# Kernel tuning notes

Measured on AMD Instinct MI355X. Metric: run time of the kernel, lower is better.

Reference implementation:

```python
import jax, jax.numpy as jnp
import numpy as np

NODE_DIM, MSG_DIM, PROP_DIM, HIDDEN = 64, 64, 32, 128
V, T, S = 10000, 8, 16


def setup_inputs() -> dict:
    key = jax.random.key(0)
    ks = jax.random.split(key, 8)
    in_dim = NODE_DIM + MSG_DIM + 1 + PROP_DIM  # concat width of the attn MLP
    return {
        "h_t": jax.random.normal(ks[0], (V, NODE_DIM), dtype=jnp.float32),
        "messages": jax.random.normal(ks[1], (V, T, S, MSG_DIM), dtype=jnp.float32),
        "tau_values": jax.random.uniform(ks[2], (T,), dtype=jnp.float32),
        "theta": jax.random.normal(ks[3], (V, PROP_DIM), dtype=jnp.float32),
        "W1": jax.random.normal(ks[4], (in_dim, HIDDEN), dtype=jnp.float32) * 0.02,
        "b1": jnp.zeros((HIDDEN,), dtype=jnp.float32),
        "W2": jax.random.normal(ks[5], (HIDDEN, 1), dtype=jnp.float32) * 0.02,
        "b2": jnp.zeros((1,), dtype=jnp.float32),
    }


def reference(h_t, messages, tau_values, theta, W1, b1, W2, b2):
    # Equivalent to concat([h_exp, messages, tau_exp, theta_exp]) @ W1:
    # split W1 by input block and sum the partial projections, avoiding the
    # materialized (V, T, S, node+msg+1+prop) broadcast-concat tensor.
    Wh = W1[:NODE_DIM]                                  # (node_dim, H)
    Wm = W1[NODE_DIM:NODE_DIM + MSG_DIM]                # (msg_dim, H)
    Wt = W1[NODE_DIM + MSG_DIM]                         # (H,) -- the tau row
    Wp = W1[NODE_DIM + MSG_DIM + 1:]                    # (prop_dim, H)

    hidden = (
        jnp.einsum("vtsd,dh->vtsh", messages, Wm)       # (V, T, S, H)
        + (h_t @ Wh)[:, None, None, :]                  # broadcast over T, S
        + tau_values[None, :, None, None] * Wt[None, None, None, :]
        + (theta @ Wp)[:, None, None, :]
        + b1
    )
    hidden = jax.nn.relu(hidden)
    logits = (hidden @ W2 + b2)[..., 0]                 # (V, T, S)
    return logits
```

## Files before the change

kernel.cpp:

```cpp
#include <hip/hip_runtime.h>
#include <hip/hip_bf16.h>

#define VN 10000
#define HID 128

using bf16x8 = __attribute__((ext_vector_type(8))) __bf16;
using f32x4  = __attribute__((ext_vector_type(4))) float;

__global__ __launch_bounds__(256) void prep_kernel(
    const float* __restrict__ h_t, const float* __restrict__ theta,
    const float* __restrict__ W1, const float* __restrict__ b1,
    float* __restrict__ base, __bf16* __restrict__ wmt)
{
  const int blk = blockIdx.x;
  const int tid = threadIdx.x;
  if (blk < 625) {
    __shared__ float in[16][96];
    const int v0 = blk * 16;
    {
      const float4* src = (const float4*)(h_t + (size_t)v0 * 64);
      float4 f = src[tid];
      int vl = tid >> 4, c = (tid & 15) * 4;
      in[vl][c] = f.x; in[vl][c + 1] = f.y; in[vl][c + 2] = f.z; in[vl][c + 3] = f.w;
    }
    if (tid < 128) {
      const float4* src = (const float4*)(theta + (size_t)v0 * 32);
      float4 f = src[tid];
      int vl = tid >> 3, c = 64 + (tid & 7) * 4;
      in[vl][c] = f.x; in[vl][c + 1] = f.y; in[vl][c + 2] = f.z; in[vl][c + 3] = f.w;
    }
    __syncthreads();
    const int h = tid & 127;
    const int half = tid >> 7;
    float acc[8];
    const float bb = b1[h];
    #pragma unroll
    for (int k = 0; k < 8; k++) acc[k] = bb;
    #pragma unroll 8
    for (int d = 0; d < 64; d++) {
      float w = W1[d * 128 + h];
      #pragma unroll
      for (int k = 0; k < 8; k++) acc[k] += in[2 * k + half][d] * w;
    }
    #pragma unroll 8
    for (int d = 0; d < 32; d++) {
      float w = W1[(129 + d) * 128 + h];
      #pragma unroll
      for (int k = 0; k < 8; k++) acc[k] += in[2 * k + half][64 + d] * w;
    }
    #pragma unroll
    for (int k = 0; k < 8; k++)
      base[(size_t)(v0 + 2 * k + half) * 128 + h] = acc[k];
  } else {
    int j = (blk - 625) * 256 + tid;
    int n = j >> 6, d = j & 63;
    wmt[j] = (__bf16)W1[(64 + d) * 128 + n];
  }
}

__global__ __launch_bounds__(256, 3) void main_kernel(
    const float* __restrict__ messages, const float* __restrict__ tau,
    const float* __restrict__ W1, const float* __restrict__ W2,
    const float* __restrict__ b2, const float* __restrict__ base,
    const __bf16* __restrict__ wmt, float* __restrict__ out)
{
  __shared__ float lOut[128];

  const int v = blockIdx.x;
  const int tid = threadIdx.x;
  const int w = tid >> 6;
  const int lane = tid & 63;
  const int quad = lane >> 4;
  const int l16 = lane & 15;

  const float* msg = messages + (size_t)v * 8192;
  float4 araw[2][2][2];
  #pragma unroll
  for (int mt = 0; mt < 2; mt++) {
    #pragma unroll
    for (int ks = 0; ks < 2; ks++) {
      const int m = 32 * w + mt * 16 + l16;
      const float4* p = (const float4*)(msg + m * 64 + ks * 32 + quad * 8);
      araw[mt][ks][0] = p[0];
      araw[mt][ks][1] = p[1];
    }
  }

  float bb[8], w2[8], wt[8];
  #pragma unroll
  for (int nt = 0; nt < 8; nt++) {
    const int n = nt * 16 + l16;
    bb[nt] = base[(size_t)v * 128 + n];
    w2[nt] = W2[n];
    wt[nt] = W1[128 * 128 + n];
  }
  float tv[2];
  tv[0] = tau[2 * w];
  tv[1] = tau[2 * w + 1];
  const float b2v = b2[0];

  f32x4 acc[2][8];
  #pragma unroll
  for (int mt = 0; mt < 2; mt++)
    #pragma unroll
    for (int nt = 0; nt < 8; nt++) acc[mt][nt] = (f32x4){0.f, 0.f, 0.f, 0.f};

  #pragma unroll
  for (int ks = 0; ks < 2; ks++) {
    bf16x8 b[8];
    #pragma unroll
    for (int nt = 0; nt < 8; nt++)
      b[nt] = *(const bf16x8*)&wmt[(nt * 16 + l16) * 64 + ks * 32 + quad * 8];
    #pragma unroll
    for (int mt = 0; mt < 2; mt++) {
      const float* af = (const float*)&araw[mt][ks][0];
      bf16x8 a;
      #pragma unroll
      for (int j = 0; j < 8; j++) a[j] = (__bf16)af[j];
      #pragma unroll
      for (int nt = 0; nt < 8; nt++)
        acc[mt][nt] = __builtin_amdgcn_mfma_f32_16x16x32_bf16(a, b[nt], acc[mt][nt], 0, 0, 0);
    }
  }

  #pragma unroll
  for (int mt = 0; mt < 2; mt++) {
    float ps[4] = {0.f, 0.f, 0.f, 0.f};
    #pragma unroll
    for (int nt = 0; nt < 8; nt++) {
      const float add = bb[nt] + tv[mt] * wt[nt];
      f32x4 a4 = acc[mt][nt];
      #pragma unroll
      for (int r = 0; r < 4; r++) {
        float hdn = fmaxf(a4[r] + add, 0.f);
        ps[r] += hdn * w2[nt];
      }
    }
    #pragma unroll
    for (int off = 1; off < 16; off <<= 1)
      #pragma unroll
      for (int r = 0; r < 4; r++) ps[r] += __shfl_xor(ps[r], off, 64);
    if (l16 == 0) {
      #pragma unroll
      for (int r = 0; r < 4; r++)
        lOut[32 * w + mt * 16 + quad * 4 + r] = ps[r];
    }
  }
  __syncthreads();
  if (tid < 128) out[(size_t)v * 128 + tid] = lOut[tid] + b2v;
}

extern "C" void kernel_launch(void* const* d_in, const int* in_sizes, int n_in,
                              void* d_out, int out_size, void* d_ws, size_t ws_size,
                              hipStream_t stream) {
  const float* h_t      = (const float*)d_in[0];
  const float* messages = (const float*)d_in[1];
  const float* tau      = (const float*)d_in[2];
  const float* theta    = (const float*)d_in[3];
  const float* W1       = (const float*)d_in[4];
  const float* b1       = (const float*)d_in[5];
  const float* W2       = (const float*)d_in[6];
  const float* b2       = (const float*)d_in[7];
  float* out = (float*)d_out;

  float* base = (float*)d_ws;
  __bf16* wmt = (__bf16*)((char*)d_ws + (size_t)VN * HID * sizeof(float));

  prep_kernel<<<625 + 32, 256, 0, stream>>>(h_t, theta, W1, b1, base, wmt);
  main_kernel<<<VN, 256, 0, stream>>>(messages, tau, W1, W2, b2, base, wmt, out);
}
```

Measured before the change: 472.7 us.

## Stage messages via global_load_lds and cache bf16 weights in LDS

The main kernel now streams each node's message tile straight into LDS with global_load_lds and reads the A fragments from LDS. The transposed bf16 Wm is loaded cooperatively into a padded LDS buffer, replacing strided per-lane global reads. The prep kernel uses float4 LDS stores and reads, with a 4-wide inner product. The aim is more coalesced global traffic and fewer redundant weight fetches, at the cost of about 52KB of LDS per block, which can lower occupancy, plus an added barrier.

After: 452.8 us. 1.04x faster.

```diff
diff --git a/kernel.cpp b/kernel.cpp
--- a/kernel.cpp
+++ b/kernel.cpp
@@ -6,6 +6,9 @@
 
 using bf16x8 = __attribute__((ext_vector_type(8))) __bf16;
 using f32x4  = __attribute__((ext_vector_type(4))) float;
+
+typedef const __attribute__((address_space(1))) uint32_t gbl_u32;
+typedef __attribute__((address_space(3))) uint32_t lds_u32;
 
 __global__ __launch_bounds__(256) void prep_kernel(
     const float* __restrict__ h_t, const float* __restrict__ theta,
@@ -15,19 +18,19 @@
   const int blk = blockIdx.x;
   const int tid = threadIdx.x;
   if (blk < 625) {
-    __shared__ float in[16][96];
+    __shared__ __align__(16) float in[16][96];
     const int v0 = blk * 16;
     {
       const float4* src = (const float4*)(h_t + (size_t)v0 * 64);
       float4 f = src[tid];
       int vl = tid >> 4, c = (tid & 15) * 4;
-      in[vl][c] = f.x; in[vl][c + 1] = f.y; in[vl][c + 2] = f.z; in[vl][c + 3] = f.w;
+      *(float4*)&in[vl][c] = f;
     }
     if (tid < 128) {
       const float4* src = (const float4*)(theta + (size_t)v0 * 32);
       float4 f = src[tid];
       int vl = tid >> 3, c = 64 + (tid & 7) * 4;
-      in[vl][c] = f.x; in[vl][c + 1] = f.y; in[vl][c + 2] = f.z; in[vl][c + 3] = f.w;
+      *(float4*)&in[vl][c] = f;
     }
     __syncthreads();
     const int h = tid & 127;
@@ -36,17 +39,31 @@
     const float bb = b1[h];
     #pragma unroll
     for (int k = 0; k < 8; k++) acc[k] = bb;
-    #pragma unroll 8
-    for (int d = 0; d < 64; d++) {
-      float w = W1[d * 128 + h];
-      #pragma unroll
-      for (int k = 0; k < 8; k++) acc[k] += in[2 * k + half][d] * w;
-    }
-    #pragma unroll 8
-    for (int d = 0; d < 32; d++) {
-      float w = W1[(129 + d) * 128 + h];
-      #pragma unroll
-      for (int k = 0; k < 8; k++) acc[k] += in[2 * k + half][64 + d] * w;
+    #pragma unroll 4
+    for (int dc = 0; dc < 16; dc++) {
+      const int d = 4 * dc;
+      float w0 = W1[(d + 0) * 128 + h];
+      float w1 = W1[(d + 1) * 128 + h];
+      float w2 = W1[(d + 2) * 128 + h];
+      float w3 = W1[(d + 3) * 128 + h];
+      #pragma unroll
+      for (int k = 0; k < 8; k++) {
+        float4 iv = *(const float4*)&in[2 * k + half][d];
+        acc[k] += iv.x * w0 + iv.y * w1 + iv.z * w2 + iv.w * w3;
+      }
+    }
+    #pragma unroll 4
+    for (int dc = 0; dc < 8; dc++) {
+      const int d = 4 * dc;
+      float w0 = W1[(129 + d + 0) * 128 + h];
+      float w1 = W1[(129 + d + 1) * 128 + h];
+      float w2 = W1[(129 + d + 2) * 128 + h];
+      float w3 = W1[(129 + d + 3) * 128 + h];
+      #pragma unroll
+      for (int k = 0; k < 8; k++) {
+        float4 iv = *(const float4*)&in[2 * k + half][64 + d];
+        acc[k] += iv.x * w0 + iv.y * w1 + iv.z * w2 + iv.w * w3;
+      }
     }
     #pragma unroll
     for (int k = 0; k < 8; k++)
@@ -64,7 +81,9 @@
     const float* __restrict__ b2, const float* __restrict__ base,
     const __bf16* __restrict__ wmt, float* __restrict__ out)
 {
-  __shared__ float lOut[128];
+  __shared__ __align__(16) unsigned char lds[33280 + 18432 + 512];
+  __bf16* lB = (__bf16*)(lds + 33280);
+  float* lOut = (float*)(lds + 33280 + 18432);
 
   const int v = blockIdx.x;
   const int tid = threadIdx.x;
@@ -74,31 +93,44 @@
   const int l16 = lane & 15;
 
   const float* msg = messages + (size_t)v * 8192;
-  float4 araw[2][2][2];
-  #pragma unroll
-  for (int mt = 0; mt < 2; mt++) {
-    #pragma unroll
-    for (int ks = 0; ks < 2; ks++) {
-      const int m = 32 * w + mt * 16 + l16;
-      const float4* p = (const float4*)(msg + m * 64 + ks * 32 + quad * 8);
-      araw[mt][ks][0] = p[0];
-      araw[mt][ks][1] = p[1];
-    }
-  }
-
-  float bb[8], w2[8], wt[8];
+
+  uint4 breg[4];
+  {
+    const uint4* bsrc = (const uint4*)wmt;
+    #pragma unroll
+    for (int j = 0; j < 4; j++) breg[j] = bsrc[j * 256 + tid];
+  }
+
+  #pragma unroll
+  for (int j = 0; j < 8; j++) {
+    const float* g = msg + (32 * w + 4 * j) * 64 + lane * 4;
+    __builtin_amdgcn_global_load_lds((gbl_u32*)g,
+                                     (lds_u32*)(lds + w * 8320 + j * 1040),
+                                     16, 0, 0);
+  }
+
+  float bb[8], w2v[8], wtv[8];
   #pragma unroll
   for (int nt = 0; nt < 8; nt++) {
     const int n = nt * 16 + l16;
-    bb[nt] = base[(size_t)v * 128 + n];
-    w2[nt] = W2[n];
-    wt[nt] = W1[128 * 128 + n];
+    bb[nt]  = base[(size_t)v * 128 + n];
+    w2v[nt] = W2[n];
+    wtv[nt] = W1[128 * 128 + n];
   }
   float tv[2];
   tv[0] = tau[2 * w];
   tv[1] = tau[2 * w + 1];
   const float b2v = b2[0];
 
+  #pragma unroll
+  for (int j = 0; j < 4; j++) {
+    int idx = j * 256 + tid;
+    int r = idx >> 3, c = (idx & 7) * 8;
+    *(uint4*)&lB[r * 72 + c] = breg[j];
+  }
+
+  __syncthreads();
+
   f32x4 acc[2][8];
   #pragma unroll
   for (int mt = 0; mt < 2; mt++)
@@ -110,13 +142,16 @@
     bf16x8 b[8];
     #pragma unroll
     for (int nt = 0; nt < 8; nt++)
-      b[nt] = *(const bf16x8*)&wmt[(nt * 16 + l16) * 64 + ks * 32 + quad * 8];
+      b[nt] = *(const bf16x8*)&lB[(nt * 16 + l16) * 72 + ks * 32 + quad * 8];
     #pragma unroll
     for (int mt = 0; mt < 2; mt++) {
-      const float* af = (const float*)&araw[mt][ks][0];
+      const int rr = mt * 16 + l16;
+      const float4* ap = (const float4*)(lds + w * 8320 + (rr >> 2) * 1040 +
+                                         (rr & 3) * 256 + (ks * 32 + quad * 8) * 4);
+      float4 f0 = ap[0], f1 = ap[1];
       bf16x8 a;
-      #pragma unroll
-      for (int j = 0; j < 8; j++) a[j] = (__bf16)af[j];
+      a[0] = (__bf16)f0.x; a[1] = (__bf16)f0.y; a[2] = (__bf16)f0.z; a[3] = (__bf16)f0.w;
+      a[4] = (__bf16)f1.x; a[5] = (__bf16)f1.y; a[6] = (__bf16)f1.z; a[7] = (__bf16)f1.w;
       #pragma unroll
       for (int nt = 0; nt < 8; nt++)
         acc[mt][nt] = __builtin_amdgcn_mfma_f32_16x16x32_bf16(a, b[nt], acc[mt][nt], 0, 0, 0);
@@ -128,12 +163,12 @@
     float ps[4] = {0.f, 0.f, 0.f, 0.f};
     #pragma unroll
     for (int nt = 0; nt < 8; nt++) {
-      const float add = bb[nt] + tv[mt] * wt[nt];
+      const float add = bb[nt] + tv[mt] * wtv[nt];
       f32x4 a4 = acc[mt][nt];
       #pragma unroll
       for (int r = 0; r < 4; r++) {
         float hdn = fmaxf(a4[r] + add, 0.f);
-        ps[r] += hdn * w2[nt];
+        ps[r] += hdn * w2v[nt];
       }
     }
     #pragma unroll
```
